# Kernel tuning notes

Hardware: AMD Instinct MI355X
Metric: run time of the kernel (lower is better)

## Reference

```python
import jax, jax.numpy as jnp
import numpy as np

D_MODEL = 1024
N_EXPERTS = 8
TOP_K = 2
LN_EPS = 1e-5


def setup_inputs() -> dict:
    key = jax.random.key(0)
    ks = jax.random.split(key, 8)
    B, S, d, E = 2, 2048, D_MODEL, N_EXPERTS
    f = 2 * d
    s_in = 0.02
    return {
        "x": jax.random.normal(ks[0], (B, S, d), jnp.float32),
        "Wg": jax.random.normal(ks[1], (d, E), jnp.float32) * s_in,
        "bg": jnp.zeros((E,), jnp.float32),
        "W1": jax.random.normal(ks[2], (E, d, f), jnp.float32) * s_in,
        "b1": jnp.zeros((E, f), jnp.float32),
        "W2": jax.random.normal(ks[3], (E, f, d), jnp.float32) * s_in,
        "b2": jnp.zeros((E, d), jnp.float32),
        "gamma": jnp.ones((d,), jnp.float32),
        "beta": jnp.zeros((d,), jnp.float32),
    }


def reference(x, Wg, bg, W1, b1, W2, b2, gamma, beta):
    # Gating + top-k routing (softmax over the selected top-k logits only)
    logits = jnp.einsum("bsd,de->bse", x, Wg) + bg            # [B,S,E]
    topk_vals, topk_idx = jax.lax.top_k(logits, TOP_K)         # [B,S,K]
    topk_w = jax.nn.softmax(topk_vals, axis=-1)                # [B,S,K]

    # Expert MLPs evaluated densely for all experts (dropout is identity in eval)
    h = jax.nn.relu(jnp.einsum("bsd,edf->bsef", x, W1) + b1)   # [B,S,E,2d]
    eo = jnp.einsum("bsef,efd->bsed", h, W2) + b2              # [B,S,E,d]

    # Gather the top-k experts' outputs per token and combine with gate weights
    sel = jnp.take_along_axis(eo, topk_idx[..., None], axis=2)  # [B,S,K,d]
    mixed = jnp.sum(sel * topk_w[..., None], axis=2)            # [B,S,d]

    # Residual + LayerNorm
    y = mixed + x
    mu = jnp.mean(y, axis=-1, keepdims=True)
    var = jnp.mean(jnp.square(y - mu), axis=-1, keepdims=True)
    return gamma * (y - mu) * jax.lax.rsqrt(var + LN_EPS) + beta
```

## Files before the change

### kernel.cpp

```cpp
#include <hip/hip_runtime.h>


typedef unsigned short ushort_t;
typedef short short8 __attribute__((ext_vector_type(8)));
typedef float f32x4 __attribute__((ext_vector_type(4)));

#define T_TOKENS 4096
#define DMODEL 1024
#define FFN 2048
#define NEXP 8
#define MAXSLOTS 9216
#define GATE_BLOCKS 256
#define TOK_PER_BLK 16

__device__ __forceinline__ ushort_t f2bf(float f) {
    unsigned u = __float_as_uint(f);
    return (ushort_t)((u + 0x7fffu + ((u >> 16) & 1u)) >> 16);
}
__device__ __forceinline__ float bflo(unsigned packed) {
    return __uint_as_float(packed << 16);
}
__device__ __forceinline__ float bfhi(unsigned packed) {
    return __uint_as_float(packed & 0xffff0000u);
}

__device__ __forceinline__ void gload_lds16(const void* g, void* l) {
    __builtin_amdgcn_global_load_lds(
        (const __attribute__((address_space(1))) unsigned int*)g,
        (__attribute__((address_space(3))) unsigned int*)l,
        16, 0, 0);
}

__global__ __launch_bounds__(256) void gate_kernel(
    const float* __restrict__ x, const float* __restrict__ Wg,
    const float* __restrict__ bg,
    int* __restrict__ top_idx, float* __restrict__ top_w,
    int* __restrict__ blk_hist)
{
    __shared__ int hist[NEXP];
    const int tid = threadIdx.x, lane = tid & 63, w = tid >> 6;
    if (tid < NEXP) hist[tid] = 0;
    __syncthreads();

    float wreg[16][8];
    #pragma unroll
    for (int i = 0; i < 16; i++) {
        const float4* wp = (const float4*)&Wg[(i * 64 + lane) * 8];
        float4 a = wp[0], b = wp[1];
        wreg[i][0] = a.x; wreg[i][1] = a.y; wreg[i][2] = a.z; wreg[i][3] = a.w;
        wreg[i][4] = b.x; wreg[i][5] = b.y; wreg[i][6] = b.z; wreg[i][7] = b.w;
    }
    float bgv[8];
    #pragma unroll
    for (int e = 0; e < 8; e++) bgv[e] = bg[e];

    const int t0 = blockIdx.x * TOK_PER_BLK + w * 4;
    #pragma unroll 1
    for (int it = 0; it < 4; it++) {
        int t = t0 + it;
        const float* xr = x + (size_t)t * DMODEL;
        float acc[8] = {0.f,0.f,0.f,0.f,0.f,0.f,0.f,0.f};
        #pragma unroll
        for (int i = 0; i < 16; i++) {
            float xv = xr[i * 64 + lane];
            #pragma unroll
            for (int e = 0; e < 8; e++) acc[e] += xv * wreg[i][e];
        }
        #pragma unroll
        for (int off = 32; off > 0; off >>= 1) {
            #pragma unroll
            for (int e = 0; e < 8; e++) acc[e] += __shfl_down(acc[e], off);
        }
        if (lane == 0) {
            float l[8];
            #pragma unroll
            for (int e = 0; e < 8; e++) l[e] = acc[e] + bgv[e];
            int i0 = 0; float v0 = l[0];
            #pragma unroll
            for (int e = 1; e < 8; e++) if (l[e] > v0) { v0 = l[e]; i0 = e; }
            int i1 = -1; float v1 = -1e30f;
            #pragma unroll
            for (int e = 0; e < 8; e++) if (e != i0 && l[e] > v1) { v1 = l[e]; i1 = e; }
            float eg = expf(v1 - v0);
            float den = 1.f + eg;
            int p0 = atomicAdd(&hist[i0], 1);
            int p1 = atomicAdd(&hist[i1], 1);
            top_idx[2 * t]     = i0 | (p0 << 4);
            top_idx[2 * t + 1] = i1 | (p1 << 4);
            top_w[2 * t]     = 1.f / den;
            top_w[2 * t + 1] = eg / den;
        }
    }
    __syncthreads();
    if (tid < NEXP) blk_hist[blockIdx.x * NEXP + tid] = hist[tid];
}

__global__ __launch_bounds__(512) void scan_kernel(
    const int* __restrict__ blk_hist, int* __restrict__ blk_base,
    int* __restrict__ offs)
{
    __shared__ int cnt[NEXP];
    const int tid = threadIdx.x, lane = tid & 63, e = tid >> 6;
    int carry = 0;
    #pragma unroll
    for (int r = 0; r < GATE_BLOCKS / 64; r++) {
        int b = r * 64 + lane;
        int orig = blk_hist[b * NEXP + e];
        int v = orig;
        #pragma unroll
        for (int off = 1; off < 64; off <<= 1) {
            int u = __shfl_up(v, off);
            if (lane >= off) v += u;
        }
        blk_base[b * NEXP + e] = carry + v - orig;
        carry += __shfl(v, 63);
    }
    if (lane == 0) cnt[e] = carry;
    __syncthreads();
    if (tid == 0) {
        int cum = 0;
        for (int ee = 0; ee < NEXP; ee++) {
            offs[ee] = cum;
            cum += (cnt[ee] + 127) & ~127;
        }
        offs[NEXP] = cum;
    }
}

__global__ __launch_bounds__(256) void scatter_gather_kernel(
    const float* __restrict__ x, const int* __restrict__ top_idx,
    const int* __restrict__ offs, const int* __restrict__ blk_base,
    int* __restrict__ slot_of, ushort_t* __restrict__ Xg)
{
    const int t = blockIdx.x, tid = threadIdx.x;
    __shared__ int slots[2];
    if (tid < 2) {
        int v = top_idx[2 * t + tid];
        int e = v & 15, pos = v >> 4;
        int gb = t / TOK_PER_BLK;
        int slot = offs[e] + blk_base[gb * NEXP + e] + pos;
        slot_of[2 * t + tid] = slot;
        slots[tid] = slot;
    }
    __syncthreads();
    float4 xv = ((const float4*)(x + (size_t)t * DMODEL))[tid];
    uint2 pk;
    pk.x = f2bf(xv.x) | ((unsigned)f2bf(xv.y) << 16);
    pk.y = f2bf(xv.z) | ((unsigned)f2bf(xv.w) << 16);
    ((uint2*)(Xg + (size_t)slots[0] * DMODEL))[tid] = pk;
    ((uint2*)(Xg + (size_t)slots[1] * DMODEL))[tid] = pk;
}

__global__ __launch_bounds__(256) void transpose_kernel(
    const float* __restrict__ W1, const float* __restrict__ W2,
    ushort_t* __restrict__ W1T, ushort_t* __restrict__ W2T)
{
    __shared__ ushort_t tile[64][68];
    int b = blockIdx.x;
    const float* s; ushort_t* d; int R, C, rt, ct;
    if (b < 4096) {
        int e = b >> 9, t = b & 511;
        rt = t >> 5; ct = t & 31;
        s = W1 + (size_t)e * DMODEL * FFN;
        d = W1T + (size_t)e * DMODEL * FFN;
        R = DMODEL; C = FFN;
    } else {
        b -= 4096;
        int e = b >> 9, t = b & 511;
        rt = t >> 4; ct = t & 15;
        s = W2 + (size_t)e * DMODEL * FFN;
        d = W2T + (size_t)e * DMODEL * FFN;
        R = FFN; C = DMODEL;
    }
    int r0 = rt * 64, c0 = ct * 64;
    int fc = threadIdx.x & 15, rp = threadIdx.x >> 4;
    #pragma unroll
    for (int p = 0; p < 4; p++) {
        int r = p * 16 + rp;
        float4 v = *(const float4*)&s[(size_t)(r0 + r) * C + c0 + fc * 4];
        uint2 pk;
        pk.x = f2bf(v.x) | ((unsigned)f2bf(v.y) << 16);
        pk.y = f2bf(v.z) | ((unsigned)f2bf(v.w) << 16);
        *(uint2*)&tile[r][fc * 4] = pk;
    }
    __syncthreads();
    #pragma unroll
    for (int p = 0; p < 4; p++) {
        int c = p * 16 + rp;
        int rb = fc * 4;
        uint2 pk;
        pk.x = tile[rb + 0][c] | ((unsigned)tile[rb + 1][c] << 16);
        pk.y = tile[rb + 2][c] | ((unsigned)tile[rb + 3][c] << 16);
        *(uint2*)&d[(size_t)(c0 + c) * R + r0 + rb] = pk;
    }
}

template <int K, int N, bool RELU>
__global__ __launch_bounds__(256) void expert_gemm(
    const ushort_t* __restrict__ A,
    const ushort_t* __restrict__ Bt,
    const float* __restrict__ bias,
    ushort_t* __restrict__ Cout,
    const int* __restrict__ offs)
{
    const int e  = blockIdx.x;
    const int nt = blockIdx.y;
    const int mt = blockIdx.z;
    const int off_e = offs[e];
    const int Mpad  = offs[e + 1] - off_e;
    if (mt * 128 >= Mpad) return;

    __shared__ __align__(16) ushort_t As[128 * 32];
    __shared__ __align__(16) ushort_t Bs[128 * 32];

    const int tid  = threadIdx.x;
    const int lane = tid & 63;
    const int w    = tid >> 6;
    const int quad = lane >> 4;
    const int r16  = lane & 15;
    const int lrow = lane >> 2;
    const int lk   = (((lane & 3) ^ ((lane >> 3) & 3))) * 8;

    const size_t arow0 = (size_t)(off_e + mt * 128);
    const ushort_t* aS0 = A + (arow0 + (size_t)(2 * w + 0) * 16 + lrow) * K + lk;
    const ushort_t* aS1 = A + (arow0 + (size_t)(2 * w + 1) * 16 + lrow) * K + lk;
    const ushort_t* Bte = Bt + (size_t)e * N * K;
    const ushort_t* bS0 = Bte + ((size_t)(nt * 128 + (2 * w + 0) * 16 + lrow)) * K + lk;
    const ushort_t* bS1 = Bte + ((size_t)(nt * 128 + (2 * w + 1) * 16 + lrow)) * K + lk;
    ushort_t* aD0 = &As[(2 * w + 0) * 512];
    ushort_t* aD1 = &As[(2 * w + 1) * 512];
    ushort_t* bD0 = &Bs[(2 * w + 0) * 512];
    ushort_t* bD1 = &Bs[(2 * w + 1) * 512];

    const int wm = (w >> 1) * 64;
    const int wn = (w & 1) * 64;
    const int sw = ((r16 >> 1) & 3) ^ quad;

    f32x4 acc[4][4];
    #pragma unroll
    for (int i = 0; i < 4; i++)
        #pragma unroll
        for (int j = 0; j < 4; j++)
            acc[i][j] = (f32x4){0.f, 0.f, 0.f, 0.f};

    for (int k0 = 0; k0 < K; k0 += 32) {
        gload_lds16(aS0 + k0, aD0);
        gload_lds16(aS1 + k0, aD1);
        gload_lds16(bS0 + k0, bD0);
        gload_lds16(bS1 + k0, bD1);
        __syncthreads();
        short8 af[4], bfr[4];
        #pragma unroll
        for (int i = 0; i < 4; i++)
            af[i] = *(const short8*)&As[(wm + i * 16 + r16) * 32 + sw * 8];
        #pragma unroll
        for (int j = 0; j < 4; j++)
            bfr[j] = *(const short8*)&Bs[(wn + j * 16 + r16) * 32 + sw * 8];
        #pragma unroll
        for (int i = 0; i < 4; i++)
            #pragma unroll
            for (int j = 0; j < 4; j++)
                acc[i][j] = __builtin_amdgcn_mfma_f32_16x16x32_bf16(
                    af[i], bfr[j], acc[i][j], 0, 0, 0);
        __syncthreads();
    }

    const float* be = bias + (size_t)e * N;
    #pragma unroll
    for (int i = 0; i < 4; i++) {
        #pragma unroll
        for (int j = 0; j < 4; j++) {
            int n = nt * 128 + wn + j * 16 + r16;
            float bv = be[n];
            #pragma unroll
            for (int r = 0; r < 4; r++) {
                int m = mt * 128 + wm + i * 16 + quad * 4 + r;
                float v = acc[i][j][r] + bv;
                if (RELU) v = v > 0.f ? v : 0.f;
                Cout[(size_t)(off_e + m) * N + n] = f2bf(v);
            }
        }
    }
}

__global__ __launch_bounds__(256) void ln_kernel(
    const float* __restrict__ x, const ushort_t* __restrict__ O,
    const int* __restrict__ slot_of, const float* __restrict__ top_w,
    const float* __restrict__ gamma, const float* __restrict__ beta,
    float* __restrict__ out)
{
    int t = blockIdx.x, tid = threadIdx.x;
    int s0 = slot_of[2 * t], s1 = slot_of[2 * t + 1];
    float w0 = top_w[2 * t], w1 = top_w[2 * t + 1];
    float4 xv = ((const float4*)(x + (size_t)t * DMODEL))[tid];
    uint2 a = ((const uint2*)(O + (size_t)s0 * DMODEL))[tid];
    uint2 b = ((const uint2*)(O + (size_t)s1 * DMODEL))[tid];

    float y[4];
    y[0] = xv.x + w0 * bflo(a.x) + w1 * bflo(b.x);
    y[1] = xv.y + w0 * bfhi(a.x) + w1 * bfhi(b.x);
    y[2] = xv.z + w0 * bflo(a.y) + w1 * bflo(b.y);
    y[3] = xv.w + w0 * bfhi(a.y) + w1 * bfhi(b.y);

    float s = y[0] + y[1] + y[2] + y[3];
    float sq = y[0]*y[0] + y[1]*y[1] + y[2]*y[2] + y[3]*y[3];
    __shared__ float red[2][4];
    #pragma unroll
    for (int off = 32; off > 0; off >>= 1) {
        s += __shfl_down(s, off);
        sq += __shfl_down(sq, off);
    }
    int lane = tid & 63, wv = tid >> 6;
    if (lane == 0) { red[0][wv] = s; red[1][wv] = sq; }
    __syncthreads();
    if (tid == 0) {
        float S = red[0][0] + red[0][1] + red[0][2] + red[0][3];
        float SQ = red[1][0] + red[1][1] + red[1][2] + red[1][3];
        float mu = S * (1.f / DMODEL);
        float var = SQ * (1.f / DMODEL) - mu * mu;
        red[0][0] = mu;
        red[1][0] = rsqrtf(var + 1e-5f);
    }
    __syncthreads();
    float mu = red[0][0], inv = red[1][0];
    float4 gv = ((const float4*)gamma)[tid];
    float4 bv = ((const float4*)beta)[tid];
    float4 ov;
    ov.x = gv.x * (y[0] - mu) * inv + bv.x;
    ov.y = gv.y * (y[1] - mu) * inv + bv.y;
    ov.z = gv.z * (y[2] - mu) * inv + bv.z;
    ov.w = gv.w * (y[3] - mu) * inv + bv.w;
    ((float4*)(out + (size_t)t * DMODEL))[tid] = ov;
}

extern "C" void kernel_launch(void* const* d_in, const int* in_sizes, int n_in,
                              void* d_out, int out_size, void* d_ws, size_t ws_size,
                              hipStream_t stream)
{
    const float* x     = (const float*)d_in[0];
    const float* Wg    = (const float*)d_in[1];
    const float* bg    = (const float*)d_in[2];
    const float* W1    = (const float*)d_in[3];
    const float* b1    = (const float*)d_in[4];
    const float* W2    = (const float*)d_in[5];
    const float* b2    = (const float*)d_in[6];
    const float* gamma = (const float*)d_in[7];
    const float* beta  = (const float*)d_in[8];
    float* out = (float*)d_out;

    char* ws = (char*)d_ws;
    size_t o = 0;
    auto alloc = [&](size_t bytes) {
        size_t r = o;
        o = (o + bytes + 255) & ~(size_t)255;
        return r;
    };
    size_t o_offs    = alloc((NEXP + 1) * 4);
    size_t o_topidx  = alloc((size_t)T_TOKENS * 2 * 4);
    size_t o_topw    = alloc((size_t)T_TOKENS * 2 * 4);
    size_t o_slotof  = alloc((size_t)T_TOKENS * 2 * 4);
    size_t o_bhist   = alloc((size_t)GATE_BLOCKS * NEXP * 4);
    size_t o_bbase   = alloc((size_t)GATE_BLOCKS * NEXP * 4);
    size_t o_w1t     = alloc((size_t)NEXP * DMODEL * FFN * 2);
    size_t o_w2t     = alloc((size_t)NEXP * DMODEL * FFN * 2);
    size_t o_xg      = alloc((size_t)MAXSLOTS * DMODEL * 2);
    size_t o_h       = alloc((size_t)MAXSLOTS * FFN * 2);
    size_t o_obuf    = alloc((size_t)MAXSLOTS * DMODEL * 2);
    (void)ws_size; (void)in_sizes; (void)n_in; (void)out_size;

    int*      offs     = (int*)(ws + o_offs);
    int*      top_idx  = (int*)(ws + o_topidx);
    float*    top_w    = (float*)(ws + o_topw);
    int*      slot_of  = (int*)(ws + o_slotof);
    int*      blk_hist = (int*)(ws + o_bhist);
    int*      blk_base = (int*)(ws + o_bbase);
    ushort_t* W1T      = (ushort_t*)(ws + o_w1t);
    ushort_t* W2T      = (ushort_t*)(ws + o_w2t);
    ushort_t* Xg       = (ushort_t*)(ws + o_xg);
    ushort_t* H        = (ushort_t*)(ws + o_h);
    ushort_t* Obuf     = (ushort_t*)(ws + o_obuf);

    gate_kernel<<<GATE_BLOCKS, 256, 0, stream>>>(x, Wg, bg, top_idx, top_w, blk_hist);
    transpose_kernel<<<8192, 256, 0, stream>>>(W1, W2, W1T, W2T);
    scan_kernel<<<1, 512, 0, stream>>>(blk_hist, blk_base, offs);
    scatter_gather_kernel<<<T_TOKENS, 256, 0, stream>>>(x, top_idx, offs, blk_base, slot_of, Xg);
    expert_gemm<DMODEL, FFN, true>
        <<<dim3(NEXP, FFN / 128, 32), 256, 0, stream>>>(Xg, W1T, b1, H, offs);
    expert_gemm<FFN, DMODEL, false>
        <<<dim3(NEXP, DMODEL / 128, 32), 256, 0, stream>>>(H, W2T, b2, Obuf, offs);
    ln_kernel<<<T_TOKENS, 256, 0, stream>>>(x, Obuf, slot_of, top_w, gamma, beta, out);
}
```

Measured before the change: 316.3 us.

## Double GEMM K-tile to 64 and transpose weights in registers without LDS

The expert GEMM now stages a 64-wide K slice per iteration with an XOR swizzle over 8 chunks, so each barrier pair covers twice as many MFMAs. The aim is to halve the synchronisation and loop overhead in the main matmul. The weight transpose/convert kernel drops its shared-memory tile and does a 4x4 register transpose per thread. That removes the LDS round-trip and barrier, but global write coalescing gets worse. The larger LDS footprint in the GEMM may reduce occupancy.

```diff
diff --git a/kernel.cpp b/kernel.cpp
--- a/kernel.cpp
+++ b/kernel.cpp
@@ -155,43 +155,37 @@
     const float* __restrict__ W1, const float* __restrict__ W2,
     ushort_t* __restrict__ W1T, ushort_t* __restrict__ W2T)
 {
-    __shared__ ushort_t tile[64][68];
     int b = blockIdx.x;
-    const float* s; ushort_t* d; int R, C, rt, ct;
+    const float* s; ushort_t* d; int Rs, Cs, rt, ct;
     if (b < 4096) {
         int e = b >> 9, t = b & 511;
         rt = t >> 5; ct = t & 31;
         s = W1 + (size_t)e * DMODEL * FFN;
         d = W1T + (size_t)e * DMODEL * FFN;
-        R = DMODEL; C = FFN;
+        Rs = DMODEL; Cs = FFN;
     } else {
         b -= 4096;
         int e = b >> 9, t = b & 511;
         rt = t >> 4; ct = t & 15;
         s = W2 + (size_t)e * DMODEL * FFN;
         d = W2T + (size_t)e * DMODEL * FFN;
-        R = FFN; C = DMODEL;
-    }
-    int r0 = rt * 64, c0 = ct * 64;
-    int fc = threadIdx.x & 15, rp = threadIdx.x >> 4;
-    #pragma unroll
-    for (int p = 0; p < 4; p++) {
-        int r = p * 16 + rp;
-        float4 v = *(const float4*)&s[(size_t)(r0 + r) * C + c0 + fc * 4];
+        Rs = FFN; Cs = DMODEL;
+    }
+    const int r0 = rt * 64, c0 = ct * 64;
+    const int ty = threadIdx.x & 15, tx = threadIdx.x >> 4;
+
+    float v[4][4];
+    #pragma unroll
+    for (int i = 0; i < 4; i++) {
+        float4 ld = *(const float4*)&s[(size_t)(r0 + ty * 4 + i) * Cs + c0 + tx * 4];
+        v[i][0] = ld.x; v[i][1] = ld.y; v[i][2] = ld.z; v[i][3] = ld.w;
+    }
+    #pragma unroll
+    for (int j = 0; j < 4; j++) {
         uint2 pk;
-        pk.x = f2bf(v.x) | ((unsigned)f2bf(v.y) << 16);
-        pk.y = f2bf(v.z) | ((unsigned)f2bf(v.w) << 16);
-        *(uint2*)&tile[r][fc * 4] = pk;
-    }
-    __syncthreads();
-    #pragma unroll
-    for (int p = 0; p < 4; p++) {
-        int c = p * 16 + rp;
-        int rb = fc * 4;
-        uint2 pk;
-        pk.x = tile[rb + 0][c] | ((unsigned)tile[rb + 1][c] << 16);
-        pk.y = tile[rb + 2][c] | ((unsigned)tile[rb + 3][c] << 16);
-        *(uint2*)&d[(size_t)(c0 + c) * R + r0 + rb] = pk;
+        pk.x = f2bf(v[0][j]) | ((unsigned)f2bf(v[1][j]) << 16);
+        pk.y = f2bf(v[2][j]) | ((unsigned)f2bf(v[3][j]) << 16);
+        *(uint2*)&d[(size_t)(c0 + tx * 4 + j) * Rs + r0 + ty * 4] = pk;
     }
 }
 
@@ -210,31 +204,27 @@
     const int Mpad  = offs[e + 1] - off_e;
     if (mt * 128 >= Mpad) return;
 
-    __shared__ __align__(16) ushort_t As[128 * 32];
-    __shared__ __align__(16) ushort_t Bs[128 * 32];
+    __shared__ __align__(16) ushort_t As[128 * 64];
+    __shared__ __align__(16) ushort_t Bs[128 * 64];
 
     const int tid  = threadIdx.x;
     const int lane = tid & 63;
     const int w    = tid >> 6;
     const int quad = lane >> 4;
     const int r16  = lane & 15;
-    const int lrow = lane >> 2;
-    const int lk   = (((lane & 3) ^ ((lane >> 3) & 3))) * 8;
+    const int srow = lane >> 3;
+    const int schunk = (lane & 7) ^ srow;
 
     const size_t arow0 = (size_t)(off_e + mt * 128);
-    const ushort_t* aS0 = A + (arow0 + (size_t)(2 * w + 0) * 16 + lrow) * K + lk;
-    const ushort_t* aS1 = A + (arow0 + (size_t)(2 * w + 1) * 16 + lrow) * K + lk;
+    const ushort_t* aBase = A + (arow0 + w * 32 + srow) * (size_t)K + schunk * 8;
     const ushort_t* Bte = Bt + (size_t)e * N * K;
-    const ushort_t* bS0 = Bte + ((size_t)(nt * 128 + (2 * w + 0) * 16 + lrow)) * K + lk;
-    const ushort_t* bS1 = Bte + ((size_t)(nt * 128 + (2 * w + 1) * 16 + lrow)) * K + lk;
-    ushort_t* aD0 = &As[(2 * w + 0) * 512];
-    ushort_t* aD1 = &As[(2 * w + 1) * 512];
-    ushort_t* bD0 = &Bs[(2 * w + 0) * 512];
-    ushort_t* bD1 = &Bs[(2 * w + 1) * 512];
+    const ushort_t* bBase = Bte + ((size_t)(nt * 128 + w * 32 + srow)) * K + schunk * 8;
+    ushort_t* aLds = &As[(w * 32) * 64];
+    ushort_t* bLds = &Bs[(w * 32) * 64];
 
     const int wm = (w >> 1) * 64;
     const int wn = (w & 1) * 64;
-    const int sw = ((r16 >> 1) & 3) ^ quad;
+    const int rk = r16 & 7;
 
     f32x4 acc[4][4];
     #pragma unroll
@@ -243,25 +233,32 @@
         for (int j = 0; j < 4; j++)
             acc[i][j] = (f32x4){0.f, 0.f, 0.f, 0.f};
 
-    for (int k0 = 0; k0 < K; k0 += 32) {
-        gload_lds16(aS0 + k0, aD0);
-        gload_lds16(aS1 + k0, aD1);
-        gload_lds16(bS0 + k0, bD0);
-        gload_lds16(bS1 + k0, bD1);
+    for (int k0 = 0; k0 < K; k0 += 64) {
+        #pragma unroll
+        for (int i = 0; i < 4; i++)
+            gload_lds16(aBase + k0 + (size_t)i * 8 * K, aLds + i * 512);
+        #pragma unroll
+        for (int i = 0; i < 4; i++)
+            gload_lds16(bBase + k0 + (size_t)i * 8 * K, bLds + i * 512);
         __syncthreads();
-        short8 af[4], bfr[4];
-        #pragma unroll
-        for (int i = 0; i < 4; i++)
-            af[i] = *(const short8*)&As[(wm + i * 16 + r16) * 32 + sw * 8];
-        #pragma unroll
-        for (int j = 0; j < 4; j++)
-            bfr[j] = *(const short8*)&Bs[(wn + j * 16 + r16) * 32 + sw * 8];
-        #pragma unroll
-        for (int i = 0; i < 4; i++)
+        #pragma unroll
+        for (int kc = 0; kc < 2; kc++) {
+            short8 af[4], bfr[4];
+            #pragma unroll
+            for (int i = 0; i < 4; i++)
+                af[i] = *(const short8*)&As[(wm + i * 16 + r16) * 64
+                                            + (((kc * 4 + quad) ^ rk)) * 8];
             #pragma unroll
             for (int j = 0; j < 4; j++)
-                acc[i][j] = __builtin_amdgcn_mfma_f32_16x16x32_bf16(
-                    af[i], bfr[j], acc[i][j], 0, 0, 0);
+                bfr[j] = *(const short8*)&Bs[(wn + j * 16 + r16) * 64
+                                             + (((kc * 4 + quad) ^ rk)) * 8];
+            #pragma unroll
+            for (int i = 0; i < 4; i++)
+                #pragma unroll
+                for (int j = 0; j < 4; j++)
+                    acc[i][j] = __builtin_amdgcn_mfma_f32_16x16x32_bf16(
+                        af[i], bfr[j], acc[i][j], 0, 0, 0);
+        }
         __syncthreads();
     }
 
```

New measurement: 337.8 us. +6.8%, slower.
